# Performance work log

Hardware: AMD Instinct MI355X
Metric: run time of the kernel (lower is better)

The kernel has to match this reference:

```python
import jax, jax.numpy as jnp
import numpy as np

HIDDEN = 4096
N_HEADS = 32
N_KV_HEADS = 8
D_HEAD = HIDDEN // N_HEADS  # 128
SEQ_LEN = 2048
ROPE_THETA = 10000.0


def _rope(t, start_index):
    # t: [L, n_heads, d_head]; rotate-half (Llama-style) RoPE
    L, _, d = t.shape
    inv_freq = 1.0 / (ROPE_THETA ** (jnp.arange(0, d, 2, dtype=jnp.float32) / d))  # [d/2]
    pos = jnp.arange(L, dtype=jnp.float32) + jnp.float32(start_index)  # [L]
    ang = pos[:, None] * inv_freq  # [L, d/2]
    cos = jnp.cos(ang)[:, None, :].astype(t.dtype)  # [L, 1, d/2]
    sin = jnp.sin(ang)[:, None, :].astype(t.dtype)
    t1, t2 = jnp.split(t, 2, axis=-1)
    return jnp.concatenate([t1 * cos - t2 * sin, t1 * sin + t2 * cos], axis=-1)


def setup_inputs() -> dict:
    key = jax.random.key(0)
    ks = jax.random.split(key, 5)
    s = 1.0 / np.sqrt(HIDDEN)
    return {
        "x": jax.random.normal(ks[0], (SEQ_LEN, HIDDEN), dtype=jnp.float32),
        "Wq": jax.random.normal(ks[1], (HIDDEN, N_HEADS * D_HEAD), dtype=jnp.float32) * s,
        "Wk": jax.random.normal(ks[2], (HIDDEN, N_KV_HEADS * D_HEAD), dtype=jnp.float32) * s,
        "Wv": jax.random.normal(ks[3], (HIDDEN, N_KV_HEADS * D_HEAD), dtype=jnp.float32) * s,
        "Wo": jax.random.normal(ks[4], (N_HEADS * D_HEAD, HIDDEN), dtype=jnp.float32) * s,
        "start_index": 0,
    }


def reference(x, Wq, Wk, Wv, Wo, start_index):
    # x: [L, hidden]; start_index==0 -> cache reset, so post-write cache == current k, v
    L, _ = x.shape
    q = (x @ Wq).reshape(L, N_HEADS, D_HEAD)
    k = (x @ Wk).reshape(L, N_KV_HEADS, D_HEAD)
    v = (x @ Wv).reshape(L, N_KV_HEADS, D_HEAD)
    q = _rope(q, start_index)
    k = _rope(k, start_index)
    # KV cache read: full cache is just [L] entries (prefill)
    S = L
    g = N_HEADS // N_KV_HEADS
    qh = q.transpose(1, 0, 2).reshape(N_KV_HEADS, g, L, D_HEAD)  # [kv, g, L, d]
    kh = k.transpose(1, 0, 2)  # [kv, S, d]
    vh = v.transpose(1, 0, 2)  # [kv, S, d]
    scale = 1.0 / np.sqrt(D_HEAD)
    scores = jnp.einsum('kgld,ksd->kgls', qh, kh) * jnp.asarray(scale, qh.dtype)
    # is_causal = (L > 1): tril(L, S) mask
    causal = jnp.tril(jnp.ones((L, S), dtype=bool))
    neg = jnp.asarray(jnp.finfo(scores.dtype).min, scores.dtype)
    scores = jnp.where(causal, scores, neg)
    attn = jax.nn.softmax(scores, axis=-1)
    out = jnp.einsum('kgls,ksd->kgld', attn, vh)  # [kv, g, L, d]
    out = out.reshape(N_HEADS, L, D_HEAD).transpose(1, 0, 2).reshape(L, N_HEADS * D_HEAD)
    return out @ Wo
```

## Files before the change

kernel.cpp:

```cpp
#include <hip/hip_runtime.h>

typedef unsigned short u16;
typedef float f32x4 __attribute__((ext_vector_type(4)));
typedef __bf16 bf16x8 __attribute__((ext_vector_type(8)));
typedef u16 u16x8 __attribute__((ext_vector_type(8)));

#define VMCNT(n) asm volatile("s_waitcnt vmcnt(" #n ")" ::: "memory")

static __device__ __forceinline__ u16 f2bf(float f) {
  union { float f; unsigned u; } v; v.f = f;
  unsigned r = v.u + 0x7fffu + ((v.u >> 16) & 1u);
  return (u16)(r >> 16);
}
static __device__ __forceinline__ float bf2f(u16 x) {
  union { unsigned u; float f; } v; v.u = (unsigned)x << 16; return v.f;
}

static __device__ __forceinline__ f32x4 mfma16(u16x8 a, u16x8 b, f32x4 c) {
  return __builtin_amdgcn_mfma_f32_16x16x32_bf16(
      __builtin_bit_cast(bf16x8, a), __builtin_bit_cast(bf16x8, b), c, 0, 0, 0);
}

static __device__ __forceinline__ void load_lds16(const void* g, void* l) {
  __builtin_amdgcn_global_load_lds(
      (const __attribute__((address_space(1))) void*)g,
      (__attribute__((address_space(3))) void*)l, 16, 0, 0);
}

__global__ void cvt_f32_bf16_swz(const float* __restrict__ in, u16* __restrict__ out, int n8) {
  int i = blockIdx.x * blockDim.x + threadIdx.x;
  if (i >= n8) return;
  int row = i >> 9;
  int j = i & 511;
  int jp = (j & ~7) | ((j & 7) ^ (row & 7));
  const float* src = in + (size_t)i * 8;
  u16x8 o;
  #pragma unroll
  for (int e = 0; e < 8; e++) o[e] = f2bf(src[e]);
  *(u16x8*)(out + ((size_t)row << 12) + jp * 8) = o;
}

__global__ __launch_bounds__(256)
void transpose_cvt(const float* __restrict__ W, u16* __restrict__ Wt, int K, int N) {
  __shared__ float tile[128][33];
  const int k0 = blockIdx.x * 128, n0 = blockIdx.y * 32;
  const int tr = threadIdx.x >> 3;
  const int tc4 = (threadIdx.x & 7) * 4;
  #pragma unroll
  for (int it = 0; it < 4; it++) {
    int kl = it * 32 + tr;
    float4 v = *(const float4*)&W[(size_t)(k0 + kl) * N + n0 + tc4];
    tile[kl][tc4] = v.x; tile[kl][tc4 + 1] = v.y;
    tile[kl][tc4 + 2] = v.z; tile[kl][tc4 + 3] = v.w;
  }
  __syncthreads();
  const int nl = threadIdx.x >> 4;
  const int dch = threadIdx.x & 15;
  #pragma unroll
  for (int it = 0; it < 2; it++) {
    int n = n0 + it * 16 + nl;
    int sch = (dch & 8) | ((dch & 7) ^ (n & 7));
    u16x8 o;
    #pragma unroll
    for (int e = 0; e < 8; e++) o[e] = f2bf(tile[sch * 8 + e][it * 16 + nl]);
    *(u16x8*)&Wt[(size_t)n * K + k0 + dch * 8] = o;
  }
}

__global__ void rope_table_k(float2* __restrict__ tab, const int* __restrict__ start, int L) {
  int i = blockIdx.x * blockDim.x + threadIdx.x;
  if (i >= L * 64) return;
  int p = i >> 6, j = i & 63;
  float inv = powf(10000.0f, -(float)j / 64.0f);
  float ang = (float)(p + start[0]) * inv;
  tab[i] = make_float2(cosf(ang), sinf(ang));
}

__global__ void rope_apply_b(const u16* __restrict__ in, int istride, int icol,
                             u16* __restrict__ outp, const float2* __restrict__ tab,
                             int total, int H, float scale, int swz) {
  int i = blockIdx.x * blockDim.x + threadIdx.x;
  if (i >= total) return;
  int j8 = (i & 7) * 8;
  int h = (i >> 3) % H;
  int p = i / (8 * H);
  const u16* base = in + (size_t)p * istride + icol + h * 128;
  u16x8 a = *(const u16x8*)(base + j8);
  u16x8 b = *(const u16x8*)(base + j8 + 64);
  u16x8 o1, o2;
  #pragma unroll
  for (int e = 0; e < 8; e++) {
    float2 cs = tab[p * 64 + j8 + e];
    float av = bf2f(a[e]), bv = bf2f(b[e]);
    o1[e] = f2bf((av * cs.x - bv * cs.y) * scale);
    o2[e] = f2bf((av * cs.y + bv * cs.x) * scale);
  }
  int c1 = i & 7;
  int cs1 = swz ? (c1 ^ (p & 7)) : c1;
  u16* ob = outp + ((size_t)p * H + h) * 128 + cs1 * 8;
  *(u16x8*)ob = o1;
  *(u16x8*)(ob + 64) = o2;
}

template<int BN, bool OUT_BF16>
__global__ __launch_bounds__(512, 2)
void gemm8p(const u16* __restrict__ A, const u16* __restrict__ Bt,
            float* __restrict__ Cf, u16* __restrict__ Cb, int N, int K, int gm) {
  constexpr int N_REP = BN / 64;
  constexpr int NHALF = N_REP / 2 > 0 ? N_REP / 2 : 1;
  constexpr int STR = 16 * NHALF;
  constexpr int BJP = (BN == 256) ? 2 : 1;
  __shared__ alignas(16) u16 As[2][256 * 64];
  __shared__ alignas(16) u16 Bs[2][BN * 64];
  const int tid = threadIdx.x;
  const int lane = tid & 63;
  const int wid = tid >> 6;
  const int ql = lane & 15, kg = lane >> 4;
  const int wr = wid >> 2, wcn = wid & 3;

  const int nb = gridDim.x;
  const int b = blockIdx.x;
  const int swz = (b & 7) * (nb >> 3) + (b >> 3);
  const int m0 = (swz % gm) * 256;
  const int n0 = (swz / gm) * BN;

  const int srow = tid >> 3, schk = tid & 7;
  const u16* abase = A + (size_t)(m0 + srow) * K + schk * 8;
  const u16* bbase = Bt + (size_t)n0 * K + schk * 8;

  auto stageA = [&](int buf, int t, int qa) {
    load_lds16(abase + (size_t)(qa * 64) * K + t * 64,
               &As[buf][((qa * 64 + srow) * 8 + schk) * 8]);
  };
  auto stageB = [&](int buf, int t, int n2, int jp) {
    int j = jp * (64 / STR) + srow / STR;
    int r = srow % STR;
    int g = j * (2 * STR) + n2 * STR + r;
    load_lds16(bbase + (size_t)g * K + t * 64,
               &Bs[buf][((n2 * (BN / 2) + jp * 64 + srow) * 8 + schk) * 8]);
  };

  f32x4 acc[8][N_REP] = {};
  u16x8 af[4][2];
  u16x8 bfr[2][NHALF][2];
  const int NT = K / 64;

  stageA(0, 0, 0); stageA(0, 0, 2);
  #pragma unroll
  for (int jp = 0; jp < BJP; jp++) stageB(0, 0, 0, jp);
  #pragma unroll
  for (int jp = 0; jp < BJP; jp++) stageB(0, 0, 1, jp);
  stageA(0, 0, 1); stageA(0, 0, 3);
  if constexpr (BN == 256) VMCNT(4); else VMCNT(3);
  __builtin_amdgcn_sched_barrier(0);
  __builtin_amdgcn_s_barrier();

  #pragma unroll 1
  for (int i = 0; i < NT / 2; i++) {
    const bool tail = (i == NT / 2 - 1);
    #pragma unroll
    for (int p = 0; p < 8; p++) {
      const int q = p & 3;
      const int m = q >> 1, n2 = q & 1;
      const int cbuf = (p < 4) ? 0 : 1;
      if (q == 0 || q == 2) {
        #pragma unroll
        for (int mi = 0; mi < 4; mi++)
          #pragma unroll
          for (int kk = 0; kk < 2; kk++) {
            int row = wr * 128 + m * 64 + mi * 16 + ql;
            int ch = ((kk << 2) | kg) ^ (ql & 7);
            af[mi][kk] = *(const u16x8*)&As[cbuf][(row * 8 + ch) * 8];
          }
      }
      if (q == 0 || q == 1) {
        #pragma unroll
        for (int ni = 0; ni < NHALF; ni++)
          #pragma unroll
          for (int kk = 0; kk < 2; kk++) {
            int R = q * (BN / 2) + wcn * STR + ni * 16 + ql;
            int ch = ((kk << 2) | kg) ^ (ql & 7);
            bfr[q][ni][kk] = *(const u16x8*)&Bs[cbuf][(R * 8 + ch) * 8];
          }
      }
      const int st = 2 * i + 1 + (p >= 4 ? 1 : 0);
      const int sbuf = st & 1;
      if (st < NT) {
        if (q == 0) { stageA(sbuf, st, 0); stageA(sbuf, st, 2); }
        else if (q == 1) {
          #pragma unroll
          for (int jp = 0; jp < BJP; jp++) stageB(sbuf, st, 0, jp);
        } else if (q == 2) {
          #pragma unroll
          for (int jp = 0; jp < BJP; jp++) stageB(sbuf, st, 1, jp);
        } else { stageA(sbuf, st, 1); stageA(sbuf, st, 3); }
      }
      if (!tail || p < 4) {
        if constexpr (BN == 256) {
          VMCNT(4);
        } else {
          if (q == 0) VMCNT(4);
          else if (q == 1) VMCNT(3);
          else if (q == 2) VMCNT(2);
          else VMCNT(3);
        }
      } else {
        if (p == 4) VMCNT(2);
        else if (p == 5) VMCNT(0);
      }
      __builtin_amdgcn_sched_barrier(0);
      __builtin_amdgcn_s_barrier();
      asm volatile("s_waitcnt lgkmcnt(0)" ::: "memory");
      __builtin_amdgcn_sched_barrier(0);
      __builtin_amdgcn_s_setprio(1);
      #pragma unroll
      for (int mi = 0; mi < 4; mi++)
        #pragma unroll
        for (int ni = 0; ni < NHALF; ni++)
          #pragma unroll
          for (int kk = 0; kk < 2; kk++)
            acc[m * 4 + mi][n2 * NHALF + ni] =
                mfma16(af[mi][kk], bfr[n2][ni][kk], acc[m * 4 + mi][n2 * NHALF + ni]);
      __builtin_amdgcn_s_setprio(0);
      __builtin_amdgcn_sched_barrier(0);
      __builtin_amdgcn_s_barrier();
    }
  }

  #pragma unroll
  for (int mi = 0; mi < 8; mi++) {
    #pragma unroll
    for (int ni = 0; ni < N_REP; ni++) {
      int row0 = m0 + wr * 128 + mi * 16 + kg * 4;
      int col = n0 + wcn * (16 * N_REP) + ni * 16 + ql;
      #pragma unroll
      for (int r = 0; r < 4; r++) {
        if constexpr (OUT_BF16)
          Cb[(size_t)(row0 + r) * N + col] = f2bf(acc[mi][ni][r]);
        else
          Cf[(size_t)(row0 + r) * N + col] = acc[mi][ni][r];
      }
    }
  }
}

__global__ __launch_bounds__(256, 2)
void attn_k(const u16* __restrict__ qr, const u16* __restrict__ kr,
            const u16* __restrict__ qkv, u16* __restrict__ out) {
  __shared__ alignas(16) u16 Kls[2][64 * 128];
  __shared__ alignas(16) u16 Vt[2][128][72];
  __shared__ alignas(16) u16 Plds[4][16][72];
  const int tid = threadIdx.x;
  const int lane = tid & 63, wave = tid >> 6;
  const int ql = lane & 15, kg = lane >> 4;
  const int h = blockIdx.y, hk = h >> 2;

  const int sl4 = (tid & 15) * 4;
  const int d0s = (tid >> 4) * 8;
  const u16* vbase = qkv + 5120 + (size_t)hk * 128 + d0s;
  const int krow_s = tid >> 4, kcol_s = (tid & 15) * 8;
  const u16* kbase = kr + (size_t)hk * 128 + (size_t)krow_s * 1024 + kcol_s;

  int cur = 0;
  #pragma unroll 1
  for (int half_idx = 0; half_idx < 2; half_idx++) {
    const int tile = half_idx ? (31 - (int)blockIdx.x) : (int)blockIdx.x;
    const int q0 = tile * 64;
    const int qw = q0 + wave * 16;
    const int nsteps = tile + 1;

    u16x8 qf[4];
    const u16* qbase = qr + ((size_t)(qw + ql) * 32 + h) * 128;
    #pragma unroll
    for (int kk = 0; kk < 4; kk++)
      qf[kk] = *(const u16x8*)(qbase + kk * 32 + kg * 8);

    f32x4 acc[8] = {};
    float m_run = -3e38f, l_run = 0.f;

    __syncthreads();
    cur = 0;
    #pragma unroll
    for (int r = 0; r < 4; r++)
      load_lds16(kbase + (size_t)r * 16 * 1024, &Kls[0][(r * 256 + tid) * 8]);
    u16x8 vreg[4];
    #pragma unroll
    for (int j = 0; j < 4; j++)
      vreg[j] = *(const u16x8*)(vbase + (size_t)(sl4 + j) * 6144);

    #pragma unroll 1
    for (int t = 0; t < nsteps; t++) {
      const int s0 = t * 64;
      #pragma unroll
      for (int e = 0; e < 8; e++) {
        ushort4 w;
        w.x = vreg[0][e]; w.y = vreg[1][e]; w.z = vreg[2][e]; w.w = vreg[3][e];
        *(ushort4*)&Vt[cur][d0s + e][sl4] = w;
      }
      __syncthreads();
      if (t + 1 < nsteps) {
        const u16* kn = kbase + (size_t)(s0 + 64) * 1024;
        #pragma unroll
        for (int r = 0; r < 4; r++)
          load_lds16(kn + (size_t)r * 16 * 1024, &Kls[cur ^ 1][(r * 256 + tid) * 8]);
        #pragma unroll
        for (int j = 0; j < 4; j++)
          vreg[j] = *(const u16x8*)(vbase + (size_t)(s0 + 64 + sl4 + j) * 6144);
      }
      f32x4 sc[4] = {};
      __builtin_amdgcn_s_setprio(1);
      #pragma unroll
      for (int sb = 0; sb < 4; sb++) {
        const u16* krow = &Kls[cur][(sb * 16 + ql) * 128];
        #pragma unroll
        for (int kk = 0; kk < 4; kk++) {
          u16x8 kf = *(const u16x8*)(krow + (((kk * 4 + kg) ^ (ql & 7)) * 8));
          sc[sb] = mfma16(kf, qf[kk], sc[sb]);
        }
      }
      __builtin_amdgcn_s_setprio(0);
      const int qg = qw + ql;
      float mt = -3e38f;
      #pragma unroll
      for (int sb = 0; sb < 4; sb++)
        #pragma unroll
        for (int r = 0; r < 4; r++) {
          int s = s0 + sb * 16 + kg * 4 + r;
          float v = (s > qg) ? -3e38f : sc[sb][r];
          sc[sb][r] = v;
          mt = fmaxf(mt, v);
        }
      mt = fmaxf(mt, __shfl_xor(mt, 16, 64));
      mt = fmaxf(mt, __shfl_xor(mt, 32, 64));
      if (!__all(mt - m_run <= 11.5f)) {
        float m_new = fmaxf(m_run, mt);
        float fco = exp2f(m_run - m_new);
        float fr[4];
        #pragma unroll
        for (int r = 0; r < 4; r++) fr[r] = __shfl(fco, (lane & 48) | (kg * 4 + r), 64);
        #pragma unroll
        for (int db = 0; db < 8; db++)
          #pragma unroll
          for (int r = 0; r < 4; r++) acc[db][r] *= fr[r];
        l_run *= fco;
        m_run = m_new;
      }
      float rs = 0.f;
      #pragma unroll
      for (int sb = 0; sb < 4; sb++)
        #pragma unroll
        for (int r = 0; r < 4; r++) {
          float e = exp2f(sc[sb][r] - m_run);
          sc[sb][r] = e;
          rs += e;
        }
      rs += __shfl_xor(rs, 16, 64);
      rs += __shfl_xor(rs, 32, 64);
      l_run += rs;
      #pragma unroll
      for (int sb = 0; sb < 4; sb++) {
        ushort4 pk;
        pk.x = f2bf(sc[sb][0]); pk.y = f2bf(sc[sb][1]);
        pk.z = f2bf(sc[sb][2]); pk.w = f2bf(sc[sb][3]);
        *(ushort4*)&Plds[wave][ql][sb * 16 + kg * 4] = pk;
      }
      __builtin_amdgcn_s_setprio(1);
      #pragma unroll
      for (int hf = 0; hf < 2; hf++) {
        u16x8 pf = *(const u16x8*)&Plds[wave][ql][hf * 32 + kg * 8];
        #pragma unroll
        for (int db = 0; db < 8; db++) {
          u16x8 vf = *(const u16x8*)&Vt[cur][db * 16 + ql][hf * 32 + kg * 8];
          acc[db] = mfma16(pf, vf, acc[db]);
        }
      }
      __builtin_amdgcn_s_setprio(0);
      cur ^= 1;
    }

    float linv[4];
    #pragma unroll
    for (int r = 0; r < 4; r++)
      linv[r] = 1.f / __shfl(l_run, (lane & 48) | (kg * 4 + r), 64);
    #pragma unroll
    for (int db = 0; db < 8; db++) {
      int d = db * 16 + ql;
      #pragma unroll
      for (int r = 0; r < 4; r++) {
        int q = qw + kg * 4 + r;
        int col = (h * 128 + d) ^ ((q & 7) << 3);
        out[(size_t)q * 4096 + col] = f2bf(acc[db][r] * linv[r]);
      }
    }
  }
}

extern "C" void kernel_launch(void* const* d_in, const int* in_sizes, int n_in,
                              void* d_out, int out_size, void* d_ws, size_t ws_size,
                              hipStream_t stream) {
  const float* x  = (const float*)d_in[0];
  const float* Wq = (const float*)d_in[1];
  const float* Wk = (const float*)d_in[2];
  const float* Wv = (const float*)d_in[3];
  const float* Wo = (const float*)d_in[4];
  const int* start = (const int*)d_in[5];

  const int L = 2048, HID = 4096, NH = 32, NKV = 8;
  const int NQ = 4096, NKVD = 1024, NF = 6144;

  char* ws = (char*)d_ws;
  size_t off = 0;
  auto alloc = [&](size_t bytes) {
    void* p = ws + off;
    off += (bytes + 255) & ~(size_t)255;
    return p;
  };
  u16* x_b   = (u16*)alloc((size_t)L * HID * 2);
  u16* Wq_t  = (u16*)alloc((size_t)NQ * HID * 2);
  u16* Wk_t  = (u16*)alloc((size_t)NKVD * HID * 2);
  u16* Wv_t  = (u16*)alloc((size_t)NKVD * HID * 2);
  u16* Wo_t  = (u16*)alloc((size_t)HID * NQ * 2);
  u16* q_r   = (u16*)alloc((size_t)L * NQ * 2);
  u16* k_r   = (u16*)alloc((size_t)L * NKVD * 2);
  float2* tab = (float2*)alloc((size_t)L * 64 * sizeof(float2));
  u16* qkv_b  = (u16*)d_out;
  u16* attn_b = Wq_t;

  const float qscale = 0.08838834764831845f * 1.4426950408889634f;

  cvt_f32_bf16_swz<<<(L * HID / 8 + 255) / 256, 256, 0, stream>>>(x, x_b, L * HID / 8);
  transpose_cvt<<<dim3(HID / 128, NQ / 32), 256, 0, stream>>>(Wq, Wq_t, HID, NQ);
  transpose_cvt<<<dim3(HID / 128, NKVD / 32), 256, 0, stream>>>(Wk, Wk_t, HID, NKVD);
  transpose_cvt<<<dim3(HID / 128, NKVD / 32), 256, 0, stream>>>(Wv, Wv_t, HID, NKVD);
  transpose_cvt<<<dim3(NQ / 128, HID / 32), 256, 0, stream>>>(Wo, Wo_t, NQ, HID);
  rope_table_k<<<(L * 64 + 255) / 256, 256, 0, stream>>>(tab, start, L);

  gemm8p<256, true><<<192, 512, 0, stream>>>(x_b, Wq_t, nullptr, qkv_b, NF, HID, 8);

  rope_apply_b<<<(L * NH * 8 + 255) / 256, 256, 0, stream>>>(qkv_b, NF, 0, q_r, tab, L * NH * 8, NH, qscale, 0);
  rope_apply_b<<<(L * NKV * 8 + 255) / 256, 256, 0, stream>>>(qkv_b, NF, NQ, k_r, tab, L * NKV * 8, NKV, 1.0f, 1);

  attn_k<<<dim3(16, NH), 256, 0, stream>>>(q_r, k_r, qkv_b, attn_b);

  gemm8p<128, false><<<256, 512, 0, stream>>>(attn_b, Wo_t, (float*)d_out, nullptr, HID, NQ, 8);
}
```

Measured before the change: 362.6 us.

## Stage contiguous B rows and coarsen GEMM prefetch waits to one per half-tile

Replaces the interleaved B-tile staging, where each wave's columns were scattered across two halves, with a plain contiguous row-block layout. The B-fragment LDS reads are re-indexed to match. All next-tile A and B loads are now issued in the first two phases of each half-iteration, with a single vmcnt(0) wait in the fourth phase instead of per-phase tuned waits and a special tail path. This simplifies the pipeline and the address math, but it front-loads memory traffic and may overlap less with compute.

```diff
diff --git a/kernel.cpp b/kernel.cpp
--- a/kernel.cpp
+++ b/kernel.cpp
@@ -108,8 +108,6 @@
             float* __restrict__ Cf, u16* __restrict__ Cb, int N, int K, int gm) {
   constexpr int N_REP = BN / 64;
   constexpr int NHALF = N_REP / 2 > 0 ? N_REP / 2 : 1;
-  constexpr int STR = 16 * NHALF;
-  constexpr int BJP = (BN == 256) ? 2 : 1;
   __shared__ alignas(16) u16 As[2][256 * 64];
   __shared__ alignas(16) u16 Bs[2][BN * 64];
   const int tid = threadIdx.x;
@@ -126,18 +124,15 @@
 
   const int srow = tid >> 3, schk = tid & 7;
   const u16* abase = A + (size_t)(m0 + srow) * K + schk * 8;
-  const u16* bbase = Bt + (size_t)n0 * K + schk * 8;
+  const u16* bbase = Bt + (size_t)(n0 + srow) * K + schk * 8;
 
   auto stageA = [&](int buf, int t, int qa) {
     load_lds16(abase + (size_t)(qa * 64) * K + t * 64,
                &As[buf][((qa * 64 + srow) * 8 + schk) * 8]);
   };
-  auto stageB = [&](int buf, int t, int n2, int jp) {
-    int j = jp * (64 / STR) + srow / STR;
-    int r = srow % STR;
-    int g = j * (2 * STR) + n2 * STR + r;
-    load_lds16(bbase + (size_t)g * K + t * 64,
-               &Bs[buf][((n2 * (BN / 2) + jp * 64 + srow) * 8 + schk) * 8]);
+  auto stageB = [&](int buf, int t, int rb) {
+    load_lds16(bbase + (size_t)(rb * 64) * K + t * 64,
+               &Bs[buf][((rb * 64 + srow) * 8 + schk) * 8]);
   };
 
   f32x4 acc[8][N_REP] = {};
@@ -147,17 +142,14 @@
 
   stageA(0, 0, 0); stageA(0, 0, 2);
   #pragma unroll
-  for (int jp = 0; jp < BJP; jp++) stageB(0, 0, 0, jp);
-  #pragma unroll
-  for (int jp = 0; jp < BJP; jp++) stageB(0, 0, 1, jp);
+  for (int rb = 0; rb < N_REP; rb++) stageB(0, 0, rb);
   stageA(0, 0, 1); stageA(0, 0, 3);
-  if constexpr (BN == 256) VMCNT(4); else VMCNT(3);
+  VMCNT(0);
   __builtin_amdgcn_sched_barrier(0);
   __builtin_amdgcn_s_barrier();
 
   #pragma unroll 1
   for (int i = 0; i < NT / 2; i++) {
-    const bool tail = (i == NT / 2 - 1);
     #pragma unroll
     for (int p = 0; p < 8; p++) {
       const int q = p & 3;
@@ -178,36 +170,25 @@
         for (int ni = 0; ni < NHALF; ni++)
           #pragma unroll
           for (int kk = 0; kk < 2; kk++) {
-            int R = q * (BN / 2) + wcn * STR + ni * 16 + ql;
+            int R = wcn * (16 * N_REP) + n2 * (16 * NHALF) + ni * 16 + ql;
             int ch = ((kk << 2) | kg) ^ (ql & 7);
-            bfr[q][ni][kk] = *(const u16x8*)&Bs[cbuf][(R * 8 + ch) * 8];
+            bfr[n2][ni][kk] = *(const u16x8*)&Bs[cbuf][(R * 8 + ch) * 8];
           }
       }
       const int st = 2 * i + 1 + (p >= 4 ? 1 : 0);
       const int sbuf = st & 1;
       if (st < NT) {
-        if (q == 0) { stageA(sbuf, st, 0); stageA(sbuf, st, 2); }
-        else if (q == 1) {
-          #pragma unroll
-          for (int jp = 0; jp < BJP; jp++) stageB(sbuf, st, 0, jp);
-        } else if (q == 2) {
-          #pragma unroll
-          for (int jp = 0; jp < BJP; jp++) stageB(sbuf, st, 1, jp);
-        } else { stageA(sbuf, st, 1); stageA(sbuf, st, 3); }
-      }
-      if (!tail || p < 4) {
-        if constexpr (BN == 256) {
-          VMCNT(4);
-        } else {
-          if (q == 0) VMCNT(4);
-          else if (q == 1) VMCNT(3);
-          else if (q == 2) VMCNT(2);
-          else VMCNT(3);
+        if (q == 0) {
+          stageA(sbuf, st, 0); stageA(sbuf, st, 2);
+          #pragma unroll
+          for (int rb = 0; rb < N_REP / 2; rb++) stageB(sbuf, st, rb);
+        } else if (q == 1) {
+          #pragma unroll
+          for (int rb = N_REP / 2; rb < N_REP; rb++) stageB(sbuf, st, rb);
+          stageA(sbuf, st, 1); stageA(sbuf, st, 3);
         }
-      } else {
-        if (p == 4) VMCNT(2);
-        else if (p == 5) VMCNT(0);
-      }
+      }
+      if (q == 3) VMCNT(0);
       __builtin_amdgcn_sched_barrier(0);
       __builtin_amdgcn_s_barrier();
       asm volatile("s_waitcnt lgkmcnt(0)" ::: "memory");
```

Measured after the change: 376.4 us. 1.04x slower.
